# Optimization experiments

Measured on AMD Instinct MI355X. Metric: run time of the kernel, lower is better.

The kernel has to match this reference:

```python
import jax, jax.numpy as jnp
import numpy as np

B, L, H, T = 64, 4, 512, 256


def setup_inputs() -> dict:
    key = jax.random.key(0)
    ks = jax.random.split(key, 7)
    k_init = 1.0 / np.sqrt(H)  # torch LSTM default uniform init bound
    return {
        "y": jax.random.normal(ks[0], (B, H), dtype=jnp.float32),
        "h0": jax.random.normal(ks[1], (L, B, H), dtype=jnp.float32),
        "c0": jax.random.normal(ks[2], (L, B, H), dtype=jnp.float32),
        "Wih": jax.random.uniform(ks[3], (L, 4 * H, H), jnp.float32, -k_init, k_init),
        "Whh": jax.random.uniform(ks[4], (L, 4 * H, H), jnp.float32, -k_init, k_init),
        "bih": jax.random.uniform(ks[5], (L, 4 * H), jnp.float32, -k_init, k_init),
        "bhh": jax.random.uniform(ks[6], (L, 4 * H), jnp.float32, -k_init, k_init),
        "seq_len": T,
    }


def _decode(y, h0, c0, Wih, Whh, bih, bhh, seq_len):
    n_layers = Wih.shape[0]

    def step(carry, _):
        x, h, c = carry  # x: [B,H], h/c: [L,B,H]
        hs, cs = [], []
        inp = x
        for l in range(n_layers):  # fixed small layer loop
            gates = inp @ Wih[l].T + bih[l] + h[l] @ Whh[l].T + bhh[l]  # [B,4H]
            i, f, g, o = jnp.split(gates, 4, axis=-1)  # torch gate order i,f,g,o
            c_new = jax.nn.sigmoid(f) * c[l] + jax.nn.sigmoid(i) * jnp.tanh(g)
            h_new = jax.nn.sigmoid(o) * jnp.tanh(c_new)
            hs.append(h_new)
            cs.append(c_new)
            inp = h_new  # output of layer l feeds layer l+1
        return (inp, jnp.stack(hs), jnp.stack(cs)), inp

    _, ys = jax.lax.scan(step, (y, h0, c0), None, length=seq_len)  # ys: [T,B,H]
    return jnp.transpose(ys, (1, 0, 2))  # [B,T,H] == torch.cat(outputs, dim=1)


def reference(y, h0, c0, Wih, Whh, bih, bhh, seq_len):
    return _decode(y, h0, c0, Wih, Whh, bih, bhh, seq_len)
```

## Files before the change

kernel.cpp:

```cpp
#include <hip/hip_runtime.h>
#include <cmath>

#define NBLK 256
#define NTHR 1024
#define Bv 64
#define Lv 4
#define Hv 512
#define Tv 256
#define G4 2048

#define WT_OFF   0u
#define HT_OFF   (33554432u)
#define YT_OFF   (HT_OFF + 1048576u)
#define BIAS_OFF (YT_OFF + 131072u)
#define BAR_OFF  (BIAS_OFF + 32768u)

__device__ __forceinline__ float sigmoidf_(float x) {
    return 1.0f / (1.0f + __expf(-x));
}

__global__ __launch_bounds__(256) void prep_wt(const float* __restrict__ Wih,
                                               const float* __restrict__ Whh,
                                               float* __restrict__ wt) {
    int bid = blockIdx.x, tid = threadIdx.x;
    float* dst = wt + (size_t)bid * (4 * 8 * 1024);
    int k = tid * 4;
#pragma unroll
    for (int l = 0; l < 4; ++l)
#pragma unroll
        for (int col = 0; col < 8; ++col) {
            int hn = bid * 2 + (col >> 2);
            int g  = col & 3;
            const float* src = (k < 512)
                ? (Wih + ((size_t)l * G4 + g * Hv + hn) * Hv + k)
                : (Whh + ((size_t)l * G4 + g * Hv + hn) * Hv + (k - 512));
            *(float4*)(dst + (size_t)(l * 8 + col) * 1024 + k) = *(const float4*)src;
        }
}

__global__ void prep_bias(const float* __restrict__ bih, const float* __restrict__ bhh,
                          float* __restrict__ biasC) {
    int idx = blockIdx.x * 256 + threadIdx.x;
    int l = idx >> 11, gi = idx & 2047;
    int hn = gi >> 2, g = gi & 3;
    biasC[idx] = bih[l * G4 + g * Hv + hn] + bhh[l * G4 + g * Hv + hn];
}

__global__ void prep_act(const float* __restrict__ y, const float* __restrict__ h0,
                         float* __restrict__ yT, float* __restrict__ hT) {
    int idx = blockIdx.x * 256 + threadIdx.x;
    if (idx < 32768) {
        int k4 = idx >> 8, b = (idx >> 2) & 63, sub = idx & 3;
        yT[idx] = y[b * Hv + k4 * 4 + sub];
    } else if (idx < 32768 + 131072) {
        int r2 = idx - 32768;
        int l = r2 >> 15, r = r2 & 32767;
        int k4 = r >> 8, b = (r >> 2) & 63, sub = r & 3;
        hT[(size_t)(4 + l) * 32768 + r] = h0[((size_t)l * Bv + b) * Hv + k4 * 4 + sub];
    }
}

__global__ __launch_bounds__(NTHR, 4) void lstm_persist(
    const float* __restrict__ wt, const float* __restrict__ biasC,
    const float* __restrict__ yT, const float* __restrict__ c0,
    float* __restrict__ hT, float* __restrict__ out,
    int* __restrict__ bar8)
{
    const int bid = blockIdx.x;
    const int tid = threadIdx.x;
    const int b   = tid & 63;
    const int s   = __builtin_amdgcn_readfirstlane(tid >> 6);

    __shared__ float4 redA[16][64];
    __shared__ float4 redB[16][64];
    __shared__ float  cst[4][2][64];

    if (tid < 512) {
        int l = tid >> 7, hn = (tid >> 6) & 1, bb = tid & 63;
        cst[l][hn][bb] = c0[((size_t)l * Bv + bb) * Hv + bid * 2 + hn];
    }
    __syncthreads();

    const float* wbase = wt + (size_t)bid * 32768;

    for (int p = 0; p < Tv * Lv; ++p) {
        const int t = p >> 2, l = p & 3;
        const int par = t & 1, ppar = par ^ 1;

        const float* xa = (l == 0)
            ? (t == 0 ? yT : hT + (size_t)(ppar * 4 + 3) * 32768)
            : hT + (size_t)(par * 4 + (l - 1)) * 32768;
        const float* ha = hT + (size_t)(ppar * 4 + l) * 32768;

        const float* act = (s < 8) ? xa : ha;
        const unsigned long long* aq =
            (const unsigned long long*)act + (size_t)(s & 7) * 2048 + b * 2;

        float av[64];
#pragma unroll
        for (int j = 0; j < 16; ++j) {
            unsigned long long lo = __hip_atomic_load(aq + (size_t)j * 128,
                                      __ATOMIC_RELAXED, __HIP_MEMORY_SCOPE_AGENT);
            unsigned long long hi = __hip_atomic_load(aq + (size_t)j * 128 + 1,
                                      __ATOMIC_RELAXED, __HIP_MEMORY_SCOPE_AGENT);
            av[4 * j + 0] = __uint_as_float((unsigned)(lo & 0xffffffffu));
            av[4 * j + 1] = __uint_as_float((unsigned)(lo >> 32));
            av[4 * j + 2] = __uint_as_float((unsigned)(hi & 0xffffffffu));
            av[4 * j + 3] = __uint_as_float((unsigned)(hi >> 32));
        }

        const float* wrow = wbase + l * 8192 + s * 64;
        float acc[8];
#pragma unroll
        for (int col = 0; col < 8; ++col) {
            const float* wp = wrow + col * 1024;
            float sum = 0.f;
#pragma unroll
            for (int k = 0; k < 64; ++k)
                sum = fmaf(wp[k], av[k], sum);
            acc[col] = sum;
        }

        redA[s][b] = make_float4(acc[0], acc[1], acc[2], acc[3]);
        redB[s][b] = make_float4(acc[4], acc[5], acc[6], acc[7]);
        __syncthreads();

        if (tid < 128) {
            const int hn = tid >> 6;
            const float4* plane = hn ? &redB[0][0] : &redA[0][0];
            float gx = 0.f, gy = 0.f, gz = 0.f, gw = 0.f;
#pragma unroll
            for (int ss = 0; ss < 16; ++ss) {
                float4 r = plane[ss * 64 + b];
                gx += r.x; gy += r.y; gz += r.z; gw += r.w;
            }
            float4 bb4 = *(const float4*)(biasC + l * G4 + bid * 8 + hn * 4);
            float ig = sigmoidf_(gx + bb4.x);
            float fg = sigmoidf_(gy + bb4.y);
            float gv = tanhf(gz + bb4.z);
            float og = sigmoidf_(gw + bb4.w);

            float cn = fg * cst[l][hn][b] + ig * gv;
            cst[l][hn][b] = cn;
            float hv = og * tanhf(cn);

            int n = bid * 2 + hn;
            __hip_atomic_store(
                &hT[(size_t)(par * 4 + l) * 32768 + ((n >> 2) * 64 + b) * 4 + (n & 3)],
                hv, __ATOMIC_RELAXED, __HIP_MEMORY_SCOPE_AGENT);
            if (l == Lv - 1)
                out[((size_t)b * Tv + t) * Hv + n] = hv;
        }

        __syncthreads();
        if (tid == 0)
            __hip_atomic_fetch_add(&bar8[(bid & 7) * 16], 1,
                                   __ATOMIC_RELEASE, __HIP_MEMORY_SCOPE_AGENT);
        if (tid < 8) {
            const int target = 32 * (p + 1);
            while (__hip_atomic_load(&bar8[tid * 16], __ATOMIC_RELAXED,
                                     __HIP_MEMORY_SCOPE_AGENT) < target) {}
        }
        __syncthreads();
    }
}

extern "C" void kernel_launch(void* const* d_in, const int* in_sizes, int n_in,
                              void* d_out, int out_size, void* d_ws, size_t ws_size,
                              hipStream_t stream)
{
    const float* y   = (const float*)d_in[0];
    const float* h0  = (const float*)d_in[1];
    const float* c0  = (const float*)d_in[2];
    const float* Wih = (const float*)d_in[3];
    const float* Whh = (const float*)d_in[4];
    const float* bih = (const float*)d_in[5];
    const float* bhh = (const float*)d_in[6];
    float* out = (float*)d_out;

    char* ws = (char*)d_ws;
    float* wt    = (float*)(ws + WT_OFF);
    float* hT    = (float*)(ws + HT_OFF);
    float* yT    = (float*)(ws + YT_OFF);
    float* biasC = (float*)(ws + BIAS_OFF);
    int*   bar8  = (int*)(ws + BAR_OFF);

    hipMemsetAsync(ws + BAR_OFF, 0, 1024, stream);

    prep_wt<<<NBLK, 256, 0, stream>>>(Wih, Whh, wt);
    prep_bias<<<32, 256, 0, stream>>>(bih, bhh, biasC);
    prep_act<<<(32768 + 131072) / 256, 256, 0, stream>>>(y, h0, yT, hT);

    lstm_persist<<<NBLK, NTHR, 0, stream>>>(wt, biasC, yT, c0, hT, out, bar8);
}
```

Baseline: 25.00 ms.

## Double-buffer per-layer weight slices into LDS via async global-to-LDS loads

Each block now prefetches the next phase's 32KB weight slice into a double-buffered LDS region with global_load_lds while computing the current phase, and reads weights from LDS instead of global memory. The goal is to hide global weight-load latency on the serial time-step critical path. It adds 64KB of LDS per block and drops the occupancy hint from launch bounds. There is no explicit wait on the async LDS loads beyond the existing barriers, which risks ordering issues.

```diff
diff --git a/kernel.cpp b/kernel.cpp
--- a/kernel.cpp
+++ b/kernel.cpp
@@ -17,6 +17,12 @@
 
 __device__ __forceinline__ float sigmoidf_(float x) {
     return 1.0f / (1.0f + __expf(-x));
+}
+
+__device__ __forceinline__ void gload_lds16(const float* g, float* l) {
+    __builtin_amdgcn_global_load_lds(
+        (const __attribute__((address_space(1))) void*)g,
+        (__attribute__((address_space(3))) void*)l, 16, 0, 0);
 }
 
 __global__ __launch_bounds__(256) void prep_wt(const float* __restrict__ Wih,
@@ -60,32 +66,45 @@
     }
 }
 
-__global__ __launch_bounds__(NTHR, 4) void lstm_persist(
+__global__ __launch_bounds__(NTHR) void lstm_persist(
     const float* __restrict__ wt, const float* __restrict__ biasC,
     const float* __restrict__ yT, const float* __restrict__ c0,
     float* __restrict__ hT, float* __restrict__ out,
     int* __restrict__ bar8)
 {
-    const int bid = blockIdx.x;
-    const int tid = threadIdx.x;
-    const int b   = tid & 63;
-    const int s   = __builtin_amdgcn_readfirstlane(tid >> 6);
-
+    const int bid  = blockIdx.x;
+    const int tid  = threadIdx.x;
+    const int b    = tid & 63;
+    const int lane = tid & 63;
+    const int wv   = tid >> 6;
+    const int s    = __builtin_amdgcn_readfirstlane(tid >> 6);
+
+    __shared__ float  wstg[2][8192];
     __shared__ float4 redA[16][64];
     __shared__ float4 redB[16][64];
     __shared__ float  cst[4][2][64];
 
+    const float* wtB = wt + (size_t)bid * 32768;
+
+    #define STAGE(ls, bn) {                                              \
+        const float* g_ = wtB + (ls) * 8192 + wv * 512 + lane * 4;       \
+        gload_lds16(g_,       &wstg[bn][wv * 512]);                      \
+        gload_lds16(g_ + 256, &wstg[bn][wv * 512 + 256]);                \
+    }
+
     if (tid < 512) {
         int l = tid >> 7, hn = (tid >> 6) & 1, bb = tid & 63;
         cst[l][hn][bb] = c0[((size_t)l * Bv + bb) * Hv + bid * 2 + hn];
     }
+    STAGE(0, 0);
     __syncthreads();
-
-    const float* wbase = wt + (size_t)bid * 32768;
 
     for (int p = 0; p < Tv * Lv; ++p) {
         const int t = p >> 2, l = p & 3;
         const int par = t & 1, ppar = par ^ 1;
+        const int cur = p & 1;
+
+        if (p + 1 < Tv * Lv) STAGE((p + 1) & 3, cur ^ 1);
 
         const float* xa = (l == 0)
             ? (t == 0 ? yT : hT + (size_t)(ppar * 4 + 3) * 32768)
@@ -109,11 +128,11 @@
             av[4 * j + 3] = __uint_as_float((unsigned)(hi >> 32));
         }
 
-        const float* wrow = wbase + l * 8192 + s * 64;
+        const float* wl = wstg[cur] + s * 64;
         float acc[8];
 #pragma unroll
         for (int col = 0; col < 8; ++col) {
-            const float* wp = wrow + col * 1024;
+            const float* wp = wl + col * 1024;
             float sum = 0.f;
 #pragma unroll
             for (int k = 0; k < 64; ++k)
@@ -128,10 +147,11 @@
         if (tid < 128) {
             const int hn = tid >> 6;
             const float4* plane = hn ? &redB[0][0] : &redA[0][0];
+            int b2 = tid & 63;
             float gx = 0.f, gy = 0.f, gz = 0.f, gw = 0.f;
 #pragma unroll
             for (int ss = 0; ss < 16; ++ss) {
-                float4 r = plane[ss * 64 + b];
+                float4 r = plane[ss * 64 + b2];
                 gx += r.x; gy += r.y; gz += r.z; gw += r.w;
             }
             float4 bb4 = *(const float4*)(biasC + l * G4 + bid * 8 + hn * 4);
@@ -140,19 +160,19 @@
             float gv = tanhf(gz + bb4.z);
             float og = sigmoidf_(gw + bb4.w);
 
-            float cn = fg * cst[l][hn][b] + ig * gv;
-            cst[l][hn][b] = cn;
+            float cn = fg * cst[l][hn][b2] + ig * gv;
+            cst[l][hn][b2] = cn;
             float hv = og * tanhf(cn);
 
             int n = bid * 2 + hn;
             __hip_atomic_store(
-                &hT[(size_t)(par * 4 + l) * 32768 + ((n >> 2) * 64 + b) * 4 + (n & 3)],
+                &hT[(size_t)(par * 4 + l) * 32768 + ((n >> 2) * 64 + b2) * 4 + (n & 3)],
                 hv, __ATOMIC_RELAXED, __HIP_MEMORY_SCOPE_AGENT);
             if (l == Lv - 1)
-                out[((size_t)b * Tv + t) * Hv + n] = hv;
-        }
-
+                out[((size_t)b2 * Tv + t) * Hv + n] = hv;
+        }
         __syncthreads();
+
         if (tid == 0)
             __hip_atomic_fetch_add(&bar8[(bid & 7) * 16], 1,
                                    __ATOMIC_RELEASE, __HIP_MEMORY_SCOPE_AGENT);
@@ -163,6 +183,7 @@
         }
         __syncthreads();
     }
+    #undef STAGE
 }
 
 extern "C" void kernel_launch(void* const* d_in, const int* in_sizes, int n_in,
```

Measured after the change: 20.63 ms. -17.5%, faster.
